# Optimization experiments

Measured on AMD Instinct MI355X. Metric: run time of the kernel, lower is better.

Reference implementation:

```python
import jax, jax.numpy as jnp
import numpy as np

KT = 0.5
KG = 0.5

def _ln(x, g, b, eps=1e-5):
    m = x.mean(-1, keepdims=True)
    v = ((x - m) ** 2).mean(-1, keepdims=True)
    return (x - m) / jnp.sqrt(v + eps) * g + b

def _sin_pe(pos, d):
    # pos: [...] float positions -> [..., d] sinusoidal encoding
    half = d // 2
    div = jnp.exp(jnp.arange(half, dtype=jnp.float32) * jnp.float32(-np.log(10000.0) * 2.0 / d))
    ang = pos[..., None].astype(jnp.float32) * div
    return jnp.concatenate([jnp.sin(ang), jnp.cos(ang)], axis=-1)

def _geo_encode(idx, emb_qk_w, w1, b1, w2, b2, ln1_g, ln1_b, ln2_g, ln2_b):
    gd = emb_qk_w.shape[-1]
    Lg = idx.shape[-1]
    x = emb_qk_w[idx]                                   # (B, S, Lg, gd)
    x = x + _sin_pe(jnp.arange(Lg, dtype=jnp.float32), gd)
    scale = 1.0 / np.sqrt(gd)
    for i in range(w1.shape[0]):
        s = jnp.einsum('bsqd,bskd->bsqk', x, x) * scale
        a = jax.nn.softmax(s, axis=-1)
        c = jnp.einsum('bsqk,bskd->bsqd', a, x)
        x = _ln(x + c, ln1_g[i], ln1_b[i])
        h = jax.nn.relu(x @ w1[i] + b1[i]) @ w2[i] + b2[i]
        x = _ln(x + h, ln2_g[i], ln2_b[i])
    return x.mean(-2)                                   # (B, S, gd)

def _forward(src_poi, src_quadkey, padding_mask, attn_mask, tgt_poi, tgt_quadkey,
             key_padding_mask, mem_mask, data_size,
             src_time, tm, gm, emb_poi_w, emb_qk_w,
             geo_ffn_w1, geo_ffn_b1, geo_ffn_w2, geo_ffn_b2,
             geo_ln1_g, geo_ln1_b, geo_ln2_g, geo_ln2_b,
             enc_wq, enc_wk, enc_wv, enc_ffn_w1, enc_ffn_b1, enc_ffn_w2, enc_ffn_b2,
             enc_ln1_g, enc_ln1_b, enc_ln2_g, enc_ln2_b,
             dec_wq, dec_wk, dec_wv, dec_ln_g, dec_ln_b, norm_g, norm_b):
    NEG = jnp.float32(-1e9)
    L = src_poi.shape[1]
    D = norm_g.shape[0]
    geo = lambda idx: _geo_encode(idx, emb_qk_w, geo_ffn_w1, geo_ffn_b1, geo_ffn_w2,
                                  geo_ffn_b2, geo_ln1_g, geo_ln1_b, geo_ln2_g, geo_ln2_b)
    src = jnp.concatenate([emb_poi_w[src_poi], geo(src_quadkey)], axis=-1)   # (B, L, D)
    tgt = jnp.concatenate([emb_poi_w[tgt_poi], geo(tgt_quadkey)], axis=-1)   # (B, Lt, D)
    # time-aware positional encoding: continuous positions from normalized timestamps
    t0 = src_time[:, :1]; tN = src_time[:, -1:]
    pos = (src_time - t0) / (tN - t0 + 1e-9) * (L - 1)
    src = src + _sin_pe(pos, D)
    # relation matrix: threshold intervals at kt/kg, then per-batch max-inversion (vectorizes the per-i loop)
    tmc = jnp.minimum(tm, KT)
    gmc = jnp.minimum(gm, KG)
    tmc = tmc.max(axis=(1, 2), keepdims=True) - tmc
    gmc = gmc.max(axis=(1, 2), keepdims=True) - gmc
    rel = tmc + gmc                                     # (B, L, L)
    scale = 1.0 / np.sqrt(D)
    emask = attn_mask[None, :, :] | padding_mask[:, None, :]
    for i in range(enc_wq.shape[0]):                    # Interval Aware Attention Blocks
        q = src @ enc_wq[i]; k = src @ enc_wk[i]; v = src @ enc_wv[i]
        s = jnp.einsum('bqd,bkd->bqk', q, k) * scale + rel
        a = jax.nn.softmax(jnp.where(emask, NEG, s), axis=-1)
        c = jnp.einsum('bqk,bkd->bqd', a, v)
        src = _ln(src + c, enc_ln1_g[i], enc_ln1_b[i])
        h = jax.nn.relu(src @ enc_ffn_w1[i] + enc_ffn_b1[i]) @ enc_ffn_w2[i] + enc_ffn_b2[i]
        src = _ln(src + h, enc_ln2_g[i], enc_ln2_b[i])
    # target-aware decoder (eval path: last encoder state broadcast over candidates)
    mem = jnp.broadcast_to(src[:, -1:, :], tgt.shape)
    dmask = mem_mask[None, :, :] | key_padding_mask[:, None, :]
    x = tgt
    for i in range(dec_wq.shape[0]):
        q = x @ dec_wq[i]; k = mem @ dec_wk[i]; v = mem @ dec_wv[i]
        s = jnp.einsum('bqd,bkd->bqk', q, k) * scale
        a = jax.nn.softmax(jnp.where(dmask, NEG, s), axis=-1)
        c = jnp.einsum('bqk,bkd->bqd', a, v)
        x = _ln(x + c, dec_ln_g[i], dec_ln_b[i])
    out = _ln(x + mem, norm_g, norm_b)
    return jnp.sum(out * tgt, axis=-1)                  # (B, Lt) matching scores

def setup_inputs():
    key = jax.random.key(0)
    ks = iter(jax.random.split(key, 64))
    nk = lambda: next(ks)
    B, L, Lg, Lt = 512, 100, 12, 101
    n_poi, n_qk = 100000, 4096
    ed, gd = 192, 64
    D = ed + gd
    Ng, Ni, Nd = 2, 2, 1
    p = lambda *s: (jax.random.normal(nk(), s, jnp.float32) * 0.02)
    return {
        'src_poi': jax.random.randint(nk(), (B, L), 0, n_poi),
        'src_quadkey': jax.random.randint(nk(), (B, L, Lg), 0, n_qk),
        'src_time': jnp.sort(jax.random.uniform(nk(), (B, L), jnp.float32) * 1e4, axis=-1),
        'tm': jax.random.uniform(nk(), (B, L, L), jnp.float32),
        'gm': jax.random.uniform(nk(), (B, L, L), jnp.float32),
        'padding_mask': jnp.zeros((B, L), bool),
        'attn_mask': jnp.triu(jnp.ones((L, L), bool), k=1),
        'tgt_poi': jax.random.randint(nk(), (B, Lt), 0, n_poi),
        'tgt_quadkey': jax.random.randint(nk(), (B, Lt, Lg), 0, n_qk),
        'key_padding_mask': jnp.zeros((B, Lt), bool),
        'mem_mask': jnp.zeros((Lt, Lt), bool),
        'data_size': jnp.full((B,), L, jnp.int32),
        'emb_poi_w': p(n_poi, ed),
        'emb_qk_w': p(n_qk, gd),
        'geo_ffn_w1': p(Ng, gd, 2 * gd), 'geo_ffn_b1': jnp.zeros((Ng, 2 * gd)),
        'geo_ffn_w2': p(Ng, 2 * gd, gd), 'geo_ffn_b2': jnp.zeros((Ng, gd)),
        'geo_ln1_g': jnp.ones((Ng, gd)), 'geo_ln1_b': jnp.zeros((Ng, gd)),
        'geo_ln2_g': jnp.ones((Ng, gd)), 'geo_ln2_b': jnp.zeros((Ng, gd)),
        'enc_wq': p(Ni, D, D), 'enc_wk': p(Ni, D, D), 'enc_wv': p(Ni, D, D),
        'enc_ffn_w1': p(Ni, D, 2 * D), 'enc_ffn_b1': jnp.zeros((Ni, 2 * D)),
        'enc_ffn_w2': p(Ni, 2 * D, D), 'enc_ffn_b2': jnp.zeros((Ni, D)),
        'enc_ln1_g': jnp.ones((Ni, D)), 'enc_ln1_b': jnp.zeros((Ni, D)),
        'enc_ln2_g': jnp.ones((Ni, D)), 'enc_ln2_b': jnp.zeros((Ni, D)),
        'dec_wq': p(Nd, D, D), 'dec_wk': p(Nd, D, D), 'dec_wv': p(Nd, D, D),
        'dec_ln_g': jnp.ones((Nd, D)), 'dec_ln_b': jnp.zeros((Nd, D)),
        'norm_g': jnp.ones((D,)), 'norm_b': jnp.zeros((D,)),
    }

def reference(src_poi, src_quadkey, src_time, tm, gm, padding_mask, attn_mask,
              tgt_poi, tgt_quadkey, key_padding_mask, mem_mask, data_size,
              emb_poi_w, emb_qk_w,
              geo_ffn_w1, geo_ffn_b1, geo_ffn_w2, geo_ffn_b2,
              geo_ln1_g, geo_ln1_b, geo_ln2_g, geo_ln2_b,
              enc_wq, enc_wk, enc_wv, enc_ffn_w1, enc_ffn_b1, enc_ffn_w2, enc_ffn_b2,
              enc_ln1_g, enc_ln1_b, enc_ln2_g, enc_ln2_b,
              dec_wq, dec_wk, dec_wv, dec_ln_g, dec_ln_b, norm_g, norm_b):
    return _forward(src_poi, src_quadkey, padding_mask, attn_mask, tgt_poi, tgt_quadkey,
                    key_padding_mask, mem_mask, data_size,
                    src_time, tm, gm, emb_poi_w, emb_qk_w,
                    geo_ffn_w1, geo_ffn_b1, geo_ffn_w2, geo_ffn_b2,
                    geo_ln1_g, geo_ln1_b, geo_ln2_g, geo_ln2_b,
                    enc_wq, enc_wk, enc_wv, enc_ffn_w1, enc_ffn_b1, enc_ffn_w2, enc_ffn_b2,
                    enc_ln1_g, enc_ln1_b, enc_ln2_g, enc_ln2_b,
                    dec_wq, dec_wk, dec_wv, dec_ln_g, dec_ln_b, norm_g, norm_b)
```

## Files before the change

### kernel.cpp

```cpp
#include <hip/hip_runtime.h>
#include <hip/hip_bf16.h>
#include <stdint.h>

typedef unsigned short u16;
typedef unsigned int   u32;
typedef __attribute__((ext_vector_type(8))) short v8s;
typedef __attribute__((ext_vector_type(4))) float v4f;

__device__ __forceinline__ float b2f(u16 u){ return __uint_as_float(((u32)u) << 16); }
__device__ __forceinline__ float lo2f(u32 u){ return __uint_as_float(u << 16); }
__device__ __forceinline__ float hi2f(u32 u){ return __uint_as_float(u & 0xffff0000u); }
__device__ __forceinline__ u16 f2b(float f){
    u32 x = __float_as_uint(f);
    u32 r = (x + 0x7fffu + ((x >> 16) & 1u)) >> 16;
    return (u16)r;
}
__device__ __forceinline__ float ldm(const void* p, size_t i, int isbf){
    return isbf ? b2f(((const u16*)p)[i]) : ((const float*)p)[i];
}
__device__ __forceinline__ float wred_sum(float v){
    #pragma unroll
    for (int o = 32; o > 0; o >>= 1) v += __shfl_xor(v, o, 64);
    return v;
}
// ... 72 lines not shown
}

template<int ACT, int SPLIT>
__global__ __launch_bounds__(256) void gemm2_kernel(
    const u16* __restrict__ A, const u16* __restrict__ Bf,
    const u16* __restrict__ bias,
    u16* __restrict__ C0, u16* __restrict__ C1, u16* __restrict__ C2,
    int M, int N, int K)
{
    const int tid = threadIdx.x, w = tid >> 6, lane = tid & 63;
    const int wm = w >> 1, wn = w & 1;
    const int flat = blockIdx.x + gridDim.x * blockIdx.y;
    const int swz = xcd_swz(flat, gridDim.x * gridDim.y);
    const int mb = swz % gridDim.x, nb = swz / gridDim.x;
    const int m0 = mb * 128 + wm * 64;
    const int n0 = nb * 128 + wn * 64;
    const int CT = K >> 5;
    const int l15 = lane & 15, lg = lane >> 4;

    v4f acc[4][4];
    #pragma unroll
    for (int mt = 0; mt < 4; mt++)
        #pragma unroll
        for (int nt = 0; nt < 4; nt++) acc[mt][nt] = (v4f){0.f, 0.f, 0.f, 0.f};

    const u16* Arow = A + (size_t)(m0 + l15) * K + (lg << 3);
    const u16* Bbase = Bf + (((size_t)(n0 >> 4) * CT) << 9) + (lane << 3);

    for (int c = 0; c < CT; c++){
        v8s bfr[4];
        #pragma unroll
        for (int nt = 0; nt < 4; nt++)
            bfr[nt] = *(const v8s*)(Bbase + (((size_t)(nt * CT + c)) << 9));
        #pragma unroll
        for (int mt = 0; mt < 4; mt++){
            v8s af = *(const v8s*)(Arow + (size_t)(mt << 4) * K + (c << 5));
            #pragma unroll
            for (int nt = 0; nt < 4; nt++)
                acc[mt][nt] = __builtin_amdgcn_mfma_f32_16x16x32_bf16(af, bfr[nt], acc[mt][nt], 0, 0, 0);
        }
    }

    #pragma unroll
    for (int nt = 0; nt < 4; nt++){
        int colbase = n0 + (nt << 4);
        float bv = bias ? b2f(bias[colbase + l15]) : 0.f;
        u16* Cp; int cw;
        if (SPLIT){
            int nbk = colbase >> 8;
            Cp = (nbk == 0) ? C0 : (nbk == 1) ? C1 : C2;
            cw = 256;
            colbase &= 255;
        } else { Cp = C0; cw = N; }
        #pragma unroll
        for (int mt = 0; mt < 4; mt++)
            #pragma unroll
            for (int r = 0; r < 4; r++){
                int row = m0 + (mt << 4) + (lg << 2) + r;
                float v = acc[mt][nt][r] + bv;
                if (ACT) v = fmaxf(v, 0.f);
                Cp[(size_t)row * cw + colbase + l15] = f2b(v);
            }
    }
}

__global__ __launch_bounds__(256) void gemm3_kernel(
    const u16* __restrict__ A, const u16* __restrict__ Bf,
    const u16* __restrict__ bias, u16* __restrict__ SRC,
    const u16* __restrict__ g, const u16* __restrict__ bta)
{
    __shared__ float red[64][4][2];
    const int tid = threadIdx.x, w = tid >> 6, lane = tid & 63;
    const int l15 = lane & 15, lg = lane >> 4;
    const int m0 = xcd_swz(blockIdx.x, gridDim.x) * 64;
    const int n0 = w * 64;
    const int CT = 16;

    v4f acc[4][4];
    #pragma unroll
    for (int mt = 0; mt < 4; mt++)
        #pragma unroll
        for (int nt = 0; nt < 4; nt++) acc[mt][nt] = (v4f){0.f, 0.f, 0.f, 0.f};

    const u16* Arow = A + (size_t)(m0 + l15) * 512 + (lg << 3);
    const u16* Bbase = Bf + (((size_t)(n0 >> 4) * CT) << 9) + (lane << 3);

    for (int c = 0; c < CT; c++){
        v8s bfr[4];
        #pragma unroll
        for (int nt = 0; nt < 4; nt++)
            bfr[nt] = *(const v8s*)(Bbase + (((size_t)(nt * CT + c)) << 9));
        #pragma unroll
        for (int mt = 0; mt < 4; mt++){
            v8s af = *(const v8s*)(Arow + (size_t)(mt << 4) * 512 + (c << 5));
            #pragma unroll
            for (int nt = 0; nt < 4; nt++)
                acc[mt][nt] = __builtin_amdgcn_mfma_f32_16x16x32_bf16(af, bfr[nt], acc[mt][nt], 0, 0, 0);
        }
    }

    float bv[4];
    #pragma unroll
    for (int nt = 0; nt < 4; nt++) bv[nt] = b2f(bias[n0 + (nt << 4) + l15]);
    #pragma unroll
    for (int mt = 0; mt < 4; mt++){
        #pragma unroll
        for (int r = 0; r < 4; r++){
            int row = m0 + (mt << 4) + (lg << 2) + r;
            float s1 = 0.f, s2 = 0.f;
            #pragma unroll
            for (int nt = 0; nt < 4; nt++){
                int col = n0 + (nt << 4) + l15;
                float y = acc[mt][nt][r] + bv[nt] + b2f(SRC[(size_t)row * 256 + col]);
                acc[mt][nt][r] = y;
                s1 += y; s2 += y * y;
            }
            s1 = wred16_sum(s1); s2 = wred16_sum(s2);
            if (l15 == 0){
                int rr = (mt << 4) + (lg << 2) + r;
                red[rr][w][0] = s1; red[rr][w][1] = s2;
            }
        }
    }
    __syncthreads();
    float gv[4], bb[4];
    #pragma unroll
    for (int nt = 0; nt < 4; nt++){
        gv[nt] = b2f(g[n0 + (nt << 4) + l15]);
        bb[nt] = b2f(bta[n0 + (nt << 4) + l15]);
    }
    #pragma unroll
    for (int mt = 0; mt < 4; mt++){
        #pragma unroll
        for (int r = 0; r < 4; r++){
            int rr = (mt << 4) + (lg << 2) + r;
            int row = m0 + rr;
            float S1 = red[rr][0][0] + red[rr][1][0] + red[rr][2][0] + red[rr][3][0];
            float S2 = red[rr][0][1] + red[rr][1][1] + red[rr][2][1] + red[rr][3][1];
            float mu = S1 * (1.0f / 256.0f);
            float var = S2 * (1.0f / 256.0f) - mu * mu;
            float rs = rsqrtf(var + 1e-5f);
            #pragma unroll
            for (int nt = 0; nt < 4; nt++){
                int col = n0 + (nt << 4) + l15;
                SRC[(size_t)row * 256 + col] = f2b((acc[mt][nt][r] - mu) * rs * gv[nt] + bb[nt]);
            }
        }
    }
}

#define GX1(r,b) (((((r) << 7) | (b))) ^ (((r) & 7) << 4))
#define GH1(r,b) (((((r) << 8) | (b))) ^ (((r) & 7) << 4))

__global__ __launch_bounds__(64) void geo6_kernel(
    const int* __restrict__ src_qk, const int* __restrict__ tgt_qk,
    const u16* __restrict__ emb,
    const u16* __restrict__ w1f, const u16* __restrict__ b1,
    const u16* __restrict__ w2f, const u16* __restrict__ b2,
    const u16* __restrict__ ln1g, const u16* __restrict__ ln1b,
    const u16* __restrict__ ln2g, const u16* __restrict__ ln2b,
    u16* __restrict__ SRC, u16* __restrict__ TGT)
{
    __shared__ __align__(16) u16 xs[16 * 64];
    __shared__ __align__(16) u16 hs[16 * 128];
    __shared__ __align__(16) float Ps[16][20];

    int seq = blockIdx.x;
    const int* qk = src_qk;
    u16* outp = SRC;
    if (seq >= 51200){ qk = tgt_qk; outp = TGT; seq -= 51200; }

    const int lane = threadIdx.x;
    const int g = lane >> 4, m = lane & 15;

    v8s ones;
    #pragma unroll
    for (int j = 0; j < 8; j++) ones[j] = (short)0x3F80;

    {
        float dv = __expf(-(float)(lane & 31) * 0.28782313662425572f);
        const bool issin = lane < 32;
        #pragma unroll
        for (int t = 0; t < 12; t++){
            int idx = qk[seq * 12 + t];
            float ang = (float)t * dv;
            float pe = issin ? __sinf(ang) : __cosf(ang);
            xs[GX1(t, lane << 1) >> 1] = f2b(b2f(emb[idx * 64 + lane]) + pe);
        }
        #pragma unroll
        for (int r = 12; r < 16; r++) xs[GX1(r, lane << 1) >> 1] = (u16)0;
    }
    lds_fence();

    float fsum = 0.f;
    const bool isdiag = (g == (m >> 2)) && (m < 12);
    const int dr = m & 3;

    for (int layer = 0; layer < 2; layer++){
        v4f S = {0.f, 0.f, 0.f, 0.f};
        {
            v8s f0 = *(const v8s*)((const char*)xs + GX1(m, (g << 4)));
            v8s f1 = *(const v8s*)((const char*)xs + GX1(m, 64 + (g << 4)));
            S = __builtin_amdgcn_mfma_f32_16x16x32_bf16(f0, f0, S, 0, 0, 0);
            S = __builtin_amdgcn_mfma_f32_16x16x32_bf16(f1, f1, S, 0, 0, 0);
        }
        {
            float ex[4];
            #pragma unroll
            for (int r = 0; r < 4; r++) ex[r] = (m < 12) ? __expf(S[r] * 0.125f) : 0.f;
            #pragma unroll
            for (int r = 0; r < 4; r++){
                float s = wred16_sum(ex[r]);
                ex[r] = ex[r] / s;
            }
            #pragma unroll
            for (int r = 0; r < 4; r++) Ps[(g << 2) + r][m] = ex[r];
        }
        lds_fence();

        float y[12];
        {
            float xr[12];
            #pragma unroll
            for (int k = 0; k < 12; k++) xr[k] = b2f(xs[GX1(k, lane << 1) >> 1]);
            #pragma unroll
            for (int q = 0; q < 12; q++){
                float4 pa = *(const float4*)&Ps[q][0];
                float4 pb = *(const float4*)&Ps[q][4];
                float4 pc = *(const float4*)&Ps[q][8];
                float c = pa.x*xr[0]+pa.y*xr[1]+pa.z*xr[2]+pa.w*xr[3]
                        + pb.x*xr[4]+pb.y*xr[5]+pb.z*xr[6]+pb.w*xr[7]
                        + pc.x*xr[8]+pc.y*xr[9]+pc.z*xr[10]+pc.w*xr[11];
                y[q] = xr[q] + c;
                xs[GX1(q, lane << 1) >> 1] = f2b(y[q]);
            }
        }
        lds_fence();

        {
            v4f R = {0.f,0.f,0.f,0.f}, Q = {0.f,0.f,0.f,0.f};
            v8s f0 = *(const v8s*)((const char*)xs + GX1(m, (g << 4)));
            v8s f1 = *(const v8s*)((const char*)xs + GX1(m, 64 + (g << 4)));
            R = __builtin_amdgcn_mfma_f32_16x16x32_bf16(f0, ones, R, 0, 0, 0);
            R = __builtin_amdgcn_mfma_f32_16x16x32_bf16(f1, ones, R, 0, 0, 0);
            Q = __builtin_amdgcn_mfma_f32_16x16x32_bf16(f0, f0, Q, 0, 0, 0);
            Q = __builtin_amdgcn_mfma_f32_16x16x32_bf16(f1, f1, Q, 0, 0, 0);
            if (isdiag){ Ps[m][16] = R[dr]; Ps[m][17] = Q[dr]; }
        }
        lds_fence();
        {
            float g1 = b2f(ln1g[layer * 64 + lane]), bb1 = b2f(ln1b[layer * 64 + lane]);
            #pragma unroll
            for (int q = 0; q < 12; q++){
                float2 st = *(const float2*)&Ps[q][16];
                float mu = st.x * 0.015625f;
                float var = st.y * 0.015625f - mu * mu;
                xs[GX1(q, lane << 1) >> 1] = f2b((y[q] - mu) * rsqrtf(var + 1e-5f) * g1 + bb1);
            }
        }
        lds_fence();

        {
            v8s a0 = *(const v8s*)((const char*)xs + GX1(m, (g << 4)));
            v8s a1 = *(const v8s*)((const char*)xs + GX1(m, 64 + (g << 4)));
            const u16* wf1 = w1f + layer * 8192;
            #pragma unroll
            for (int nt = 0; nt < 8; nt++){
                v8s bfa = *(const v8s*)(wf1 + (((nt << 1) + 0) << 9) + (lane << 3));
                v8s bfb = *(const v8s*)(wf1 + (((nt << 1) + 1) << 9) + (lane << 3));
                v4f h = {0.f, 0.f, 0.f, 0.f};
                h = __builtin_amdgcn_mfma_f32_16x16x32_bf16(a0, bfa, h, 0, 0, 0);
                h = __builtin_amdgcn_mfma_f32_16x16x32_bf16(a1, bfb, h, 0, 0, 0);
                float bia = b2f(b1[layer * 128 + (nt << 4) + m]);
                #pragma unroll
                for (int r = 0; r < 4; r++)
                    hs[GH1((g << 2) + r, ((nt << 4) | m) << 1) >> 1] = f2b(fmaxf(h[r] + bia, 0.f));
            }
        }
        lds_fence();

        {
            v8s ha[4];
            #pragma unroll
            for (int c = 0; c < 4; c++)
                ha[c] = *(const v8s*)((const char*)hs + GH1(m, (c << 6) + (g << 4)));
            lds_fence();
            float* os = (float*)hs;
            const u16* wf2 = w2f + layer * 8192;
            #pragma unroll
            for (int nt = 0; nt < 4; nt++){
                v4f o = {0.f, 0.f, 0.f, 0.f};
                #pragma unroll
                for (int c = 0; c < 4; c++){
                    v8s bf = *(const v8s*)(wf2 + ((((nt << 2) + c) << 9) + (lane << 3)));
                    o = __builtin_amdgcn_mfma_f32_16x16x32_bf16(ha[c], bf, o, 0, 0, 0);
                }
                float bo = b2f(b2[layer * 64 + (nt << 4) + m]);
                #pragma unroll
                for (int r = 0; r < 4; r++)
                    os[((g << 2) + r) * 64 + (nt << 4) + m] = o[r] + bo;
            }
        }
        lds_fence();

        {
            const float* os = (const float*)hs;
            #pragma unroll
            for (int q = 0; q < 12; q++){
                y[q] = b2f(xs[GX1(q, lane << 1) >> 1]) + os[q * 64 + lane];
            }
            lds_fence();
            #pragma unroll
            for (int q = 0; q < 12; q++)
                xs[GX1(q, lane << 1) >> 1] = f2b(y[q]);
        }
        lds_fence();
        {
            v4f R = {0.f,0.f,0.f,0.f}, Q = {0.f,0.f,0.f,0.f};
            v8s f0 = *(const v8s*)((const char*)xs + GX1(m, (g << 4)));
            v8s f1 = *(const v8s*)((const char*)xs + GX1(m, 64 + (g << 4)));
            R = __builtin_amdgcn_mfma_f32_16x16x32_bf16(f0, ones, R, 0, 0, 0);
            R = __builtin_amdgcn_mfma_f32_16x16x32_bf16(f1, ones, R, 0, 0, 0);
            Q = __builtin_amdgcn_mfma_f32_16x16x32_bf16(f0, f0, Q, 0, 0, 0);
            Q = __builtin_amdgcn_mfma_f32_16x16x32_bf16(f1, f1, Q, 0, 0, 0);
            if (isdiag){ Ps[m][16] = R[dr]; Ps[m][17] = Q[dr]; }
        }
        lds_fence();
        {
            float g2 = b2f(ln2g[layer * 64 + lane]), bb2 = b2f(ln2b[layer * 64 + lane]);
            #pragma unroll
            for (int q = 0; q < 12; q++){
                float2 st = *(const float2*)&Ps[q][16];
                float mu = st.x * 0.015625f;
                float var = st.y * 0.015625f - mu * mu;
                float xv = (y[q] - mu) * rsqrtf(var + 1e-5f) * g2 + bb2;
                if (layer == 0) xs[GX1(q, lane << 1) >> 1] = f2b(xv);
                else            fsum += xv;
            }
        }
        lds_fence();
    }
    outp[(size_t)seq * 256 + 192 + lane] = f2b(fsum * (1.0f / 12.0f));
}

__global__ __launch_bounds__(256) void embed_src_kernel(
    const int* __restrict__ poi, const float* __restrict__ timev,
    const void* __restrict__ emb_poi, u16* __restrict__ src,
    const int* __restrict__ flag)
{
    const int bl = blockIdx.x;
    const int d  = threadIdx.x;
    const int b  = bl / 100;
    const int isbf = *flag;
    float t0 = timev[b * 100];
    float tN = timev[b * 100 + 99];
    float tv = timev[bl];
    float pos = (tv - t0) / (tN - t0 + 1e-9f) * 99.0f;
    int j = d & 127;
    float dvv = __expf(-(float)j * 0.07195578415606393f);
    float ang = pos * dvv;
    float pe = (d < 128) ? __sinf(ang) : __cosf(ang);
    size_t off = (size_t)bl * 256 + d;
    float val = (d < 192) ? ldm(emb_poi, (size_t)poi[bl] * 192 + d, isbf) : b2f(src[off]);
    src[off] = f2b(val + pe);
}

__global__ __launch_bounds__(256) void embed_tgt_kernel(
    const int* __restrict__ poi, const void* __restrict__ emb_poi,
    u16* __restrict__ tgt, int n, const int* __restrict__ flag)
{
    int i = blockIdx.x * 256 + threadIdx.x;
    if (i >= n * 192) return;
    int bt = i / 192; int d = i - bt * 192;
    tgt[(size_t)bt * 256 + d] = f2b(ldm(emb_poi, (size_t)poi[bt] * 192 + d, *flag));
}

__global__ __launch_bounds__(256) void relmax_kernel(
    const void* __restrict__ tm, const void* __restrict__ gm,
    float* __restrict__ relm, const int* __restrict__ flag)
{
    const int b = blockIdx.x, tid = threadIdx.x;
    const int isbf = *flag;
    size_t base = (size_t)b * 10000;
    float tmax = -1e30f, gmax = -1e30f;
    for (int i = tid; i < 10000; i += 256){
        tmax = fmaxf(tmax, fminf(ldm(tm, base + i, isbf), 0.5f));
        gmax = fmaxf(gmax, fminf(ldm(gm, base + i, isbf), 0.5f));
    }
    tmax = wred_max(tmax); gmax = wred_max(gmax);
    __shared__ float st[4], sg[4];
    if ((tid & 63) == 0){ st[tid >> 6] = tmax; sg[tid >> 6] = gmax; }
    __syncthreads();
    if (tid == 0){
        relm[b * 2]     = fmaxf(fmaxf(st[0], st[1]), fmaxf(st[2], st[3]));
        relm[b * 2 + 1] = fmaxf(fmaxf(sg[0], sg[1]), fmaxf(sg[2], sg[3]));
    }
}

__global__ __launch_bounds__(256) void attn_kernel(
    const u16* __restrict__ QB, const u16* __restrict__ Kg, const u16* __restrict__ Vg,
    u16* __restrict__ SRC,
    const void* __restrict__ tmp_, const void* __restrict__ gmp_,
    const float* __restrict__ relm,
    const u16* __restrict__ lng, const u16* __restrict__ lnb,
    const int* __restrict__ flag)
{
    __shared__ __align__(16) u16 KV[100][264];
    __shared__ __align__(16) u16 Amat[50][112];

    const int blk = xcd_swz(blockIdx.x, gridDim.x);
    const int b = blk >> 1, h = blk & 1;
    const int tid = threadIdx.x;
    const int w = tid >> 6, lane = tid & 63;
    const int l15 = lane & 15, lg = lane >> 4;
    const int q0 = h * 50;
    const int nk = q0 + 50;
    const int isbf = *flag;
    const float tmax = relm[b * 2], gmax = relm[b * 2 + 1];

    const u16* Vb = Vg + (size_t)b * 100 * 256;
    for (int i = tid; i < nk * 128; i += 256){
        int row = i >> 7, c2 = (i & 127) * 2;
        *(ushort2*)&KV[row][c2] = *(const ushort2*)(Vb + row * 256 + c2);
    }

    const int ntc = (h == 0) ? 4 : 7;
    const int qrow = q0 + w * 16 + l15;
    const u16* Aq = QB + ((size_t)b * 100 + (qrow < 100 ? qrow : 99)) * 256 + (lg << 3);
    const u16* Kb = Kg + (size_t)b * 100 * 256;
    v4f S[7];
    #pragma unroll
    for (int nt = 0; nt < 7; nt++) S[nt] = (v4f){0.f, 0.f, 0.f, 0.f};
    const u16* Bp[7];
    for (int nt = 0; nt < ntc; nt++){
        int kt = nt * 16 + l15;
        Bp[nt] = Kb + (size_t)(kt < 100 ? kt : 99) * 256 + (lg << 3);
    }
    for (int c = 0; c < 8; c++){
        v8s af = *(const v8s*)(Aq + (c << 5));
        for (int nt = 0; nt < ntc; nt++){
            v8s bf = *(const v8s*)(Bp[nt] + (c << 5));
            S[nt] = __builtin_amdgcn_mfma_f32_16x16x32_bf16(af, bf, S[nt], 0, 0, 0);
        }
    }

    float P[7][4];
    #pragma unroll
    for (int r = 0; r < 4; r++){
        int qrel = w * 16 + (lg << 2) + r;
        int q = q0 + qrel;
        int qc = q < 100 ? q : 99;
        size_t rbase = ((size_t)b * 100 + qc) * 100;
        float sv[7];
        float mx = -1e30f;
        for (int nt = 0; nt < ntc; nt++){
            int kt = nt * 16 + l15;
            int ktc = kt < 100 ? kt : 99;
            float rel = (tmax - fminf(ldm(tmp_, rbase + ktc, isbf), 0.5f))
                      + (gmax - fminf(ldm(gmp_, rbase + ktc, isbf), 0.5f));
            float s = S[nt][r] * 0.0625f + rel;
            if (kt > q) s = -1e30f;
            sv[nt] = s;
            mx = fmaxf(mx, s);
        }
        mx = wred16_max(mx);
        float sum = 0.f;
        for (int nt = 0; nt < ntc; nt++){ sv[nt] = __expf(sv[nt] - mx); sum += sv[nt]; }
        sum = wred16_sum(sum);
        float inv = 1.0f / sum;
        for (int nt = 0; nt < ntc; nt++) P[nt][r] = sv[nt] * inv;
    }
    #pragma unroll
    for (int r = 0; r < 4; r++){
        int qrel = w * 16 + (lg << 2) + r;
        if (qrel < 50){
            for (int nt = 0; nt < ntc; nt++)
                Amat[qrel][nt * 16 + l15] = f2b(P[nt][r]);
        }
    }
    __syncthreads();

    for (int qq = 0; qq < 13; qq++){
        const int qr = qq * 4 + w;
        const int q  = q0 + qr;
        if (qr < 50){
            float o00 = 0.f, o01 = 0.f, o10 = 0.f, o11 = 0.f;
            const int kfull = (q + 1) & ~7;
            for (int k8 = 0; k8 < (kfull >> 3); k8++){
                uint4 av = *(const uint4*)&Amat[qr][k8 * 8];
                float p[8] = { lo2f(av.x), hi2f(av.x), lo2f(av.y), hi2f(av.y),
                               lo2f(av.z), hi2f(av.z), lo2f(av.w), hi2f(av.w) };
                #pragma unroll
                for (int j = 0; j < 8; j++){
                    int k = k8 * 8 + j;
                    u32 v0 = *(const u32*)&KV[k][2 * lane];
                    u32 v1 = *(const u32*)&KV[k][128 + 2 * lane];
                    o00 += p[j] * lo2f(v0); o01 += p[j] * hi2f(v0);
                    o10 += p[j] * lo2f(v1); o11 += p[j] * hi2f(v1);
                }
            }
            for (int k = kfull; k <= q; k++){
                float a = b2f(Amat[qr][k]);
                u32 v0 = *(const u32*)&KV[k][2 * lane];
                u32 v1 = *(const u32*)&KV[k][128 + 2 * lane];
                o00 += a * lo2f(v0); o01 += a * hi2f(v0);
                o10 += a * lo2f(v1); o11 += a * hi2f(v1);
            }
            u16* Sg = SRC + ((size_t)b * 100 + q) * 256;
            u32 s0v = *(const u32*)&Sg[2 * lane];
            u32 s1v = *(const u32*)&Sg[128 + 2 * lane];
            float y0 = o00 + lo2f(s0v), y1 = o01 + hi2f(s0v);
            float y2 = o10 + lo2f(s1v), y3 = o11 + hi2f(s1v);
            float s1 = y0 + y1 + y2 + y3;
            float s2 = y0*y0 + y1*y1 + y2*y2 + y3*y3;
            s1 = wred_sum(s1); s2 = wred_sum(s2);
            float mu = s1 * (1.0f / 256.0f);
            float var = s2 * (1.0f / 256.0f) - mu * mu;
            float rs = rsqrtf(var + 1e-5f);
            u32 g0 = *(const u32*)&lng[2 * lane], g1 = *(const u32*)&lng[128 + 2 * lane];
            u32 b0 = *(const u32*)&lnb[2 * lane], b1 = *(const u32*)&lnb[128 + 2 * lane];
            ushort2 w0, w1;
            w0.x = f2b((y0 - mu) * rs * lo2f(g0) + lo2f(b0));
            w0.y = f2b((y1 - mu) * rs * hi2f(g0) + hi2f(b0));
            w1.x = f2b((y2 - mu) * rs * lo2f(g1) + lo2f(b1));
            w1.y = f2b((y3 - mu) * rs * hi2f(g1) + hi2f(b1));
            *(ushort2*)&Sg[2 * lane]       = w0;
            *(ushort2*)&Sg[128 + 2 * lane] = w1;
        }
    }
}

__global__ __launch_bounds__(256) void decv_kernel(
    const u16* __restrict__ SRC, const u16* __restrict__ wv, float* __restrict__ VS)
{
    __shared__ float sv[256];
    const int b = blockIdx.x, n = threadIdx.x;
    const u16* s = SRC + ((size_t)b * 100 + 99) * 256;
    sv[n] = b2f(s[n]);
    __syncthreads();
    float acc = 0.f;
    for (int d = 0; d < 256; d++) acc += sv[d] * b2f(wv[d * 256 + n]);
    VS[(size_t)b * 256 + n] = acc;
}

__global__ __launch_bounds__(64) void decfinal2_kernel(
    const u16* __restrict__ TGT, const u16* __restrict__ SRC,
    const float* __restrict__ VS,
    const u16* __restrict__ dlg, const u16* __restrict__ dlb,
    const u16* __restrict__ ng,  const u16* __restrict__ nb,
    void* __restrict__ outp, const int* __restrict__ flag)
{
    const int bt = blockIdx.x, lane = threadIdx.x;
    const int b = bt / 101;
    const int c4 = lane * 4;
    ushort4 tg4  = *(const ushort4*)(TGT + (size_t)bt * 256 + c4);
    ushort4 mem4 = *(const ushort4*)(SRC + ((size_t)b * 100 + 99) * 256 + c4);
    float4  vs4  = *(const float4*)(VS + (size_t)b * 256 + c4);
    float tg[4]  = { b2f(tg4.x), b2f(tg4.y), b2f(tg4.z), b2f(tg4.w) };
    float mem[4] = { b2f(mem4.x), b2f(mem4.y), b2f(mem4.z), b2f(mem4.w) };
    float vsv[4] = { vs4.x, vs4.y, vs4.z, vs4.w };
    float y[4], s1 = 0.f, s2 = 0.f;
    #pragma unroll
    for (int i = 0; i < 4; i++){ y[i] = tg[i] + vsv[i]; s1 += y[i]; s2 += y[i]*y[i]; }
    s1 = wred_sum(s1); s2 = wred_sum(s2);
    float mu1 = s1 * (1.0f / 256.0f);
    float v1 = s2 * (1.0f / 256.0f) - mu1 * mu1;
    float rs1 = rsqrtf(v1 + 1e-5f);
    ushort4 dg4 = *(const ushort4*)(dlg + c4), db4 = *(const ushort4*)(dlb + c4);
    float dg[4] = { b2f(dg4.x), b2f(dg4.y), b2f(dg4.z), b2f(dg4.w) };
    float db[4] = { b2f(db4.x), b2f(db4.y), b2f(db4.z), b2f(db4.w) };
    float y2[4], a2 = 0.f, b2s = 0.f;
    #pragma unroll
    for (int i = 0; i < 4; i++){
        float x = (y[i] - mu1) * rs1 * dg[i] + db[i];
        y2[i] = x + mem[i];
        a2 += y2[i]; b2s += y2[i]*y2[i];
    }
    a2 = wred_sum(a2); b2s = wred_sum(b2s);
    float mu2 = a2 * (1.0f / 256.0f);
    float v2 = b2s * (1.0f / 256.0f) - mu2 * mu2;
    float rs2 = rsqrtf(v2 + 1e-5f);
    ushort4 ng4 = *(const ushort4*)(ng + c4), nb4 = *(const ushort4*)(nb + c4);
    float ngv[4] = { b2f(ng4.x), b2f(ng4.y), b2f(ng4.z), b2f(ng4.w) };
    float nbv[4] = { b2f(nb4.x), b2f(nb4.y), b2f(nb4.z), b2f(nb4.w) };
    float tot = 0.f;
    #pragma unroll
    for (int i = 0; i < 4; i++){
        float o = (y2[i] - mu2) * rs2 * ngv[i] + nbv[i];
        tot += o * tg[i];
    }
    tot = wred_sum(tot);
    if (lane == 0){
        if (*flag) ((u16*)outp)[bt] = f2b(tot);
        else       ((float*)outp)[bt] = tot;
    }
}

extern "C" void kernel_launch(void* const* d_in, const int* in_sizes, int n_in,
                              void* d_out, int out_size, void* d_ws, size_t ws_size,
                              hipStream_t stream)
{
    char* ws = (char*)d_ws;
    size_t off = 0;
    auto AL = [&](size_t bytes){ size_t o = off; off += (bytes + 255) & ~(size_t)255; return o; };
    const size_t FLAGO = AL(4);
    const size_t CTIME = AL(51200 * 4);
    const size_t CEQK  = AL(262144 * 2);
    const size_t CGW1  = AL(16384 * 2), CGB1 = AL(256 * 2), CGW2 = AL(16384 * 2), CGB2 = AL(128 * 2);
    const size_t CGL1G = AL(128 * 2), CGL1B = AL(128 * 2), CGL2G = AL(128 * 2), CGL2B = AL(128 * 2);
    const size_t CEWQ  = AL(131072 * 2), CEWK = AL(131072 * 2), CEWV = AL(131072 * 2);
    const size_t CEW1  = AL(262144 * 2), CEB1 = AL(1024 * 2), CEW2 = AL(262144 * 2), CEB2 = AL(512 * 2);
    const size_t CEL1G = AL(512 * 2), CEL1B = AL(512 * 2), CEL2G = AL(512 * 2), CEL2B = AL(512 * 2);
    const size_t CDWV  = AL(65536 * 2), CDLG = AL(256 * 2), CDLB = AL(256 * 2), CNG = AL(256 * 2), CNB = AL(256 * 2);
    const size_t W1FO  = AL(16384 * 2), W2FO = AL(16384 * 2);
    const size_t QKVFO = AL(786432 * 2);
    const size_t W1FEO = AL(524288 * 2);
    const size_t W2FEO = AL(524288 * 2);
    const size_t RELMO = AL(512 * 2 * 4);
    const size_t VSO   = AL(512 * 256 * 4);
    const size_t SRCO  = AL((size_t)51200 * 256 * 2);
    const size_t TGTO  = AL((size_t)51712 * 256 * 2);
    const size_t B1O   = AL((size_t)51200 * 256 * 2);
    const size_t B2O   = AL((size_t)51200 * 256 * 2);
    const size_t B3O   = AL((size_t)51200 * 256 * 2);
    (void)ws_size; (void)in_sizes; (void)n_in; (void)out_size;

    int*   FLAG = (int*)(ws + FLAGO);
    float* CT   = (float*)(ws + CTIME);
    u16 *cEQK=(u16*)(ws+CEQK), *cGW1=(u16*)(ws+CGW1), *cGB1=(u16*)(ws+CGB1), *cGW2=(u16*)(ws+CGW2),
        *cGB2=(u16*)(ws+CGB2), *cGL1G=(u16*)(ws+CGL1G), *cGL1B=(u16*)(ws+CGL1B), *cGL2G=(u16*)(ws+CGL2G),
        *cGL2B=(u16*)(ws+CGL2B), *cEWQ=(u16*)(ws+CEWQ), *cEWK=(u16*)(ws+CEWK), *cEWV=(u16*)(ws+CEWV),
        *cEW1=(u16*)(ws+CEW1), *cEB1=(u16*)(ws+CEB1), *cEW2=(u16*)(ws+CEW2), *cEB2=(u16*)(ws+CEB2),
        *cEL1G=(u16*)(ws+CEL1G), *cEL1B=(u16*)(ws+CEL1B), *cEL2G=(u16*)(ws+CEL2G), *cEL2B=(u16*)(ws+CEL2B),
        *cDWV=(u16*)(ws+CDWV), *cDLG=(u16*)(ws+CDLG), *cDLB=(u16*)(ws+CDLB), *cNG=(u16*)(ws+CNG),
        *cNB=(u16*)(ws+CNB);
    u16* W1F   = (u16*)(ws + W1FO);
    u16* W2F   = (u16*)(ws + W2FO);
    u16* QKVF  = (u16*)(ws + QKVFO);
    u16* W1FE  = (u16*)(ws + W1FEO);
    u16* W2FE  = (u16*)(ws + W2FEO);
    float* RELM = (float*)(ws + RELMO);
    float* VS   = (float*)(ws + VSO);
    u16* SRC = (u16*)(ws + SRCO);
    u16* TGT = (u16*)(ws + TGTO);
    u16* B1  = (u16*)(ws + B1O);
    u16* B2  = (u16*)(ws + B2O);
    u16* B3  = (u16*)(ws + B3O);
    u16* Hh  = B2;

    const int* src_poi = (const int*)d_in[0];
    const int* src_qk  = (const int*)d_in[1];
    const int* tgt_poi = (const int*)d_in[7];
    const int* tgt_qk  = (const int*)d_in[8];

    probe_kernel<<<1, 64, 0, stream>>>((const u32*)d_in[38], FLAG);

    ConvArgs ca;
    const int srcidx[NSEG] = {13,14,15,16,17,18,19,20,21,22,23,24,25,26,27,28,29,30,31,32,35,36,37,38,39};
    u16* dsts[NSEG] = {cEQK,cGW1,cGB1,cGW2,cGB2,cGL1G,cGL1B,cGL2G,cGL2B,cEWQ,cEWK,cEWV,
                       cEW1,cEB1,cEW2,cEB2,cEL1G,cEL1B,cEL2G,cEL2B,cDWV,cDLG,cDLB,cNG,cNB};
    const int ns[NSEG] = {262144,16384,256,16384,128,128,128,128,128,131072,131072,131072,
                          262144,1024,262144,512,512,512,512,512,65536,256,256,256,256};
    for (int i = 0; i < NSEG; i++){ ca.src[i] = d_in[srcidx[i]]; ca.dst[i] = dsts[i]; ca.n[i] = ns[i]; }
    convert_kernel<<<dim3(1024, NSEG), 256, 0, stream>>>(ca, FLAG);
    convert_time_kernel<<<200, 256, 0, stream>>>(d_in[2], CT, FLAG);

    packfrag_kernel<<<64, 256, 0, stream>>>(cGW1, W1F, 64, 128, 2);
    packfrag_kernel<<<64, 256, 0, stream>>>(cGW2, W2F, 128, 64, 2);
    packfrag3_kernel<<<3072, 256, 0, stream>>>(cEWQ, cEWK, cEWV, QKVF);
    packfrag_kernel<<<1024, 256, 0, stream>>>(cEW1, W1FE, 256, 512, 2);
    packfrag_kernel<<<1024, 256, 0, stream>>>(cEW2, W2FE, 512, 256, 2);

    geo6_kernel<<<102912, 64, 0, stream>>>(src_qk, tgt_qk, cEQK, W1F, cGB1, W2F, cGB2,
                                           cGL1G, cGL1B, cGL2G, cGL2B, SRC, TGT);
    embed_src_kernel<<<51200, 256, 0, stream>>>(src_poi, CT, d_in[12], SRC, FLAG);
    embed_tgt_kernel<<<(51712 * 192 + 255) / 256, 256, 0, stream>>>(tgt_poi, d_in[12], TGT, 51712, FLAG);
    relmax_kernel<<<512, 256, 0, stream>>>(d_in[3], d_in[4], RELM, FLAG);

    for (int i = 0; i < 2; i++){
        gemm2_kernel<0,1><<<dim3(400, 6), 256, 0, stream>>>(SRC, QKVF + (size_t)i * 196608, nullptr,
                                                            B1, B2, B3, 51200, 768, 256);
        attn_kernel<<<1024, 256, 0, stream>>>(B1, B2, B3, SRC, d_in[3], d_in[4], RELM,
                                              cEL1G + i * 256, cEL1B + i * 256, FLAG);
        gemm2_kernel<1,0><<<dim3(400, 4), 256, 0, stream>>>(SRC, W1FE + (size_t)i * 131072, cEB1 + i * 512,
                                                            Hh, nullptr, nullptr, 51200, 512, 256);
        gemm3_kernel<<<800, 256, 0, stream>>>(Hh, W2FE + (size_t)i * 131072, cEB2 + i * 256,
                                              SRC, cEL2G + i * 256, cEL2B + i * 256);
    }

    decv_kernel<<<512, 256, 0, stream>>>(SRC, cDWV, VS);
    decfinal2_kernel<<<51712, 64, 0, stream>>>(TGT, SRC, VS, cDLG, cDLB, cNG, cNB, d_out, FLAG);
}
```

Baseline: 1.215 ms.

## Fuse geo encoder, POI embeddings and relmax into one block-dispatched kernel

Merges the geo encoder, source and target POI embedding kernels, and the relative-max reduction into a single launch, choosing the role from the block index. The source path no longer does a read-modify-write of the geo columns: the geo block adds the cosine positional term itself and the embed blocks write only the first 192 columns. This saves three kernel launches and one pass over the SRC geo slice. Relmax now runs as 512 single-wave blocks instead of 256-thread blocks, and the launch bounds gain a minimum-occupancy hint of 8.

```diff
diff --git a/kernel.cpp b/kernel.cpp
--- a/kernel.cpp
+++ b/kernel.cpp
@@ -248,248 +248,245 @@
 #define GX1(r,b) (((((r) << 7) | (b))) ^ (((r) & 7) << 4))
 #define GH1(r,b) (((((r) << 8) | (b))) ^ (((r) & 7) << 4))
 
-__global__ __launch_bounds__(64) void geo6_kernel(
+__global__ __launch_bounds__(64, 8) void fused1_kernel(
     const int* __restrict__ src_qk, const int* __restrict__ tgt_qk,
     const u16* __restrict__ emb,
     const u16* __restrict__ w1f, const u16* __restrict__ b1,
     const u16* __restrict__ w2f, const u16* __restrict__ b2,
     const u16* __restrict__ ln1g, const u16* __restrict__ ln1b,
     const u16* __restrict__ ln2g, const u16* __restrict__ ln2b,
-    u16* __restrict__ SRC, u16* __restrict__ TGT)
+    u16* __restrict__ SRC, u16* __restrict__ TGT,
+    const int* __restrict__ src_poi, const int* __restrict__ tgt_poi,
+    const void* __restrict__ emb_poi, const float* __restrict__ CTm,
+    const void* __restrict__ tm, const void* __restrict__ gm,
+    float* __restrict__ relm, const int* __restrict__ flag)
 {
     __shared__ __align__(16) u16 xs[16 * 64];
     __shared__ __align__(16) u16 hs[16 * 128];
     __shared__ __align__(16) float Ps[16][20];
 
-    int seq = blockIdx.x;
-    const int* qk = src_qk;
-    u16* outp = SRC;
-    if (seq >= 51200){ qk = tgt_qk; outp = TGT; seq -= 51200; }
-
+    const int bid = blockIdx.x;
     const int lane = threadIdx.x;
-    const int g = lane >> 4, m = lane & 15;
-
-    v8s ones;
-    #pragma unroll
-    for (int j = 0; j < 8; j++) ones[j] = (short)0x3F80;
-
-    {
-        float dv = __expf(-(float)(lane & 31) * 0.28782313662425572f);
-        const bool issin = lane < 32;
-        #pragma unroll
-        for (int t = 0; t < 12; t++){
-            int idx = qk[seq * 12 + t];
-            float ang = (float)t * dv;
-            float pe = issin ? __sinf(ang) : __cosf(ang);
-            xs[GX1(t, lane << 1) >> 1] = f2b(b2f(emb[idx * 64 + lane]) + pe);
-        }
-        #pragma unroll
-        for (int r = 12; r < 16; r++) xs[GX1(r, lane << 1) >> 1] = (u16)0;
-    }
-    lds_fence();
-
-    float fsum = 0.f;
-    const bool isdiag = (g == (m >> 2)) && (m < 12);
-    const int dr = m & 3;
-
-    for (int layer = 0; layer < 2; layer++){
-        v4f S = {0.f, 0.f, 0.f, 0.f};
+
+    if (bid < 102912){
+        int seq = bid;
+        const int* qk = src_qk;
+        u16* outp = SRC;
+        bool is_src = true;
+        if (seq >= 51200){ qk = tgt_qk; outp = TGT; seq -= 51200; is_src = false; }
+
+        const int g = lane >> 4, m = lane & 15;
+        v8s ones;
+        #pragma unroll
+        for (int j = 0; j < 8; j++) ones[j] = (short)0x3F80;
+
         {
-            v8s f0 = *(const v8s*)((const char*)xs + GX1(m, (g << 4)));
-            v8s f1 = *(const v8s*)((const char*)xs + GX1(m, 64 + (g << 4)));
-            S = __builtin_amdgcn_mfma_f32_16x16x32_bf16(f0, f0, S, 0, 0, 0);
-            S = __builtin_amdgcn_mfma_f32_16x16x32_bf16(f1, f1, S, 0, 0, 0);
-        }
-        {
-            float ex[4];
+            float dv = __expf(-(float)(lane & 31) * 0.28782313662425572f);
+            const bool issin = lane < 32;
             #pragma unroll
-            for (int r = 0; r < 4; r++) ex[r] = (m < 12) ? __expf(S[r] * 0.125f) : 0.f;
+            for (int t = 0; t < 12; t++){
+                int idx = qk[seq * 12 + t];
+                float ang = (float)t * dv;
+                float pe = issin ? __sinf(ang) : __cosf(ang);
+                xs[GX1(t, lane << 1) >> 1] = f2b(b2f(emb[idx * 64 + lane]) + pe);
+            }
             #pragma unroll
-            for (int r = 0; r < 4; r++){
-                float s = wred16_sum(ex[r]);
-                ex[r] = ex[r] / s;
-            }
-            #pragma unroll
-            for (int r = 0; r < 4; r++) Ps[(g << 2) + r][m] = ex[r];
+            for (int r = 12; r < 16; r++) xs[GX1(r, lane << 1) >> 1] = (u16)0;
         }
         lds_fence();
 
-        float y[12];
-        {
-            float xr[12];
-            #pragma unroll
-            for (int k = 0; k < 12; k++) xr[k] = b2f(xs[GX1(k, lane << 1) >> 1]);
-            #pragma unroll
-            for (int q = 0; q < 12; q++){
-                float4 pa = *(const float4*)&Ps[q][0];
-                float4 pb = *(const float4*)&Ps[q][4];
-                float4 pc = *(const float4*)&Ps[q][8];
-                float c = pa.x*xr[0]+pa.y*xr[1]+pa.z*xr[2]+pa.w*xr[3]
-                        + pb.x*xr[4]+pb.y*xr[5]+pb.z*xr[6]+pb.w*xr[7]
-                        + pc.x*xr[8]+pc.y*xr[9]+pc.z*xr[10]+pc.w*xr[11];
-                y[q] = xr[q] + c;
-                xs[GX1(q, lane << 1) >> 1] = f2b(y[q]);
-            }
-        }
-        lds_fence();
-
-        {
-            v4f R = {0.f,0.f,0.f,0.f}, Q = {0.f,0.f,0.f,0.f};
-            v8s f0 = *(const v8s*)((const char*)xs + GX1(m, (g << 4)));
-            v8s f1 = *(const v8s*)((const char*)xs + GX1(m, 64 + (g << 4)));
-            R = __builtin_amdgcn_mfma_f32_16x16x32_bf16(f0, ones, R, 0, 0, 0);
-            R = __builtin_amdgcn_mfma_f32_16x16x32_bf16(f1, ones, R, 0, 0, 0);
-            Q = __builtin_amdgcn_mfma_f32_16x16x32_bf16(f0, f0, Q, 0, 0, 0);
-            Q = __builtin_amdgcn_mfma_f32_16x16x32_bf16(f1, f1, Q, 0, 0, 0);
-            if (isdiag){ Ps[m][16] = R[dr]; Ps[m][17] = Q[dr]; }
-        }
-        lds_fence();
-        {
-            float g1 = b2f(ln1g[layer * 64 + lane]), bb1 = b2f(ln1b[layer * 64 + lane]);
-            #pragma unroll
-            for (int q = 0; q < 12; q++){
-                float2 st = *(const float2*)&Ps[q][16];
-                float mu = st.x * 0.015625f;
-                float var = st.y * 0.015625f - mu * mu;
-                xs[GX1(q, lane << 1) >> 1] = f2b((y[q] - mu) * rsqrtf(var + 1e-5f) * g1 + bb1);
-            }
-        }
-        lds_fence();
-
-        {
-            v8s a0 = *(const v8s*)((const char*)xs + GX1(m, (g << 4)));
-            v8s a1 = *(const v8s*)((const char*)xs + GX1(m, 64 + (g << 4)));
-            const u16* wf1 = w1f + layer * 8192;
-            #pragma unroll
-            for (int nt = 0; nt < 8; nt++){
-                v8s bfa = *(const v8s*)(wf1 + (((nt << 1) + 0) << 9) + (lane << 3));
-                v8s bfb = *(const v8s*)(wf1 + (((nt << 1) + 1) << 9) + (lane << 3));
-                v4f h = {0.f, 0.f, 0.f, 0.f};
-                h = __builtin_amdgcn_mfma_f32_16x16x32_bf16(a0, bfa, h, 0, 0, 0);
-                h = __builtin_amdgcn_mfma_f32_16x16x32_bf16(a1, bfb, h, 0, 0, 0);
-                float bia = b2f(b1[layer * 128 + (nt << 4) + m]);
-                #pragma unroll
-                for (int r = 0; r < 4; r++)
-                    hs[GH1((g << 2) + r, ((nt << 4) | m) << 1) >> 1] = f2b(fmaxf(h[r] + bia, 0.f));
-            }
-        }
-        lds_fence();
-
-        {
-            v8s ha[4];
-            #pragma unroll
-            for (int c = 0; c < 4; c++)
-                ha[c] = *(const v8s*)((const char*)hs + GH1(m, (c << 6) + (g << 4)));
-            lds_fence();
-            float* os = (float*)hs;
-            const u16* wf2 = w2f + layer * 8192;
-            #pragma unroll
-            for (int nt = 0; nt < 4; nt++){
-                v4f o = {0.f, 0.f, 0.f, 0.f};
-                #pragma unroll
-                for (int c = 0; c < 4; c++){
-                    v8s bf = *(const v8s*)(wf2 + ((((nt << 2) + c) << 9) + (lane << 3)));
-                    o = __builtin_amdgcn_mfma_f32_16x16x32_bf16(ha[c], bf, o, 0, 0, 0);
+        float fsum = 0.f;
+        const bool isdiag = (g == (m >> 2)) && (m < 12);
+        const int dr = m & 3;
+
+        for (int layer = 0; layer < 2; layer++){
+            v4f S = {0.f, 0.f, 0.f, 0.f};
+            {
+                v8s f0 = *(const v8s*)((const char*)xs + GX1(m, (g << 4)));
+                v8s f1 = *(const v8s*)((const char*)xs + GX1(m, 64 + (g << 4)));
+                S = __builtin_amdgcn_mfma_f32_16x16x32_bf16(f0, f0, S, 0, 0, 0);
+                S = __builtin_amdgcn_mfma_f32_16x16x32_bf16(f1, f1, S, 0, 0, 0);
+            }
+            {
+                float ex[4];
+                #pragma unroll
+                for (int r = 0; r < 4; r++) ex[r] = (m < 12) ? __expf(S[r] * 0.125f) : 0.f;
+                #pragma unroll
+                for (int r = 0; r < 4; r++){
+                    float s = wred16_sum(ex[r]);
+                    ex[r] = ex[r] / s;
                 }
-                float bo = b2f(b2[layer * 64 + (nt << 4) + m]);
-                #pragma unroll
-                for (int r = 0; r < 4; r++)
-                    os[((g << 2) + r) * 64 + (nt << 4) + m] = o[r] + bo;
-            }
-        }
-        lds_fence();
-
-        {
-            const float* os = (const float*)hs;
-            #pragma unroll
-            for (int q = 0; q < 12; q++){
-                y[q] = b2f(xs[GX1(q, lane << 1) >> 1]) + os[q * 64 + lane];
-            }
-            lds_fence();
-            #pragma unroll
-            for (int q = 0; q < 12; q++)
-                xs[GX1(q, lane << 1) >> 1] = f2b(y[q]);
-        }
-        lds_fence();
-        {
-            v4f R = {0.f,0.f,0.f,0.f}, Q = {0.f,0.f,0.f,0.f};
-            v8s f0 = *(const v8s*)((const char*)xs + GX1(m, (g << 4)));
-            v8s f1 = *(const v8s*)((const char*)xs + GX1(m, 64 + (g << 4)));
-            R = __builtin_amdgcn_mfma_f32_16x16x32_bf16(f0, ones, R, 0, 0, 0);
-            R = __builtin_amdgcn_mfma_f32_16x16x32_bf16(f1, ones, R, 0, 0, 0);
-            Q = __builtin_amdgcn_mfma_f32_16x16x32_bf16(f0, f0, Q, 0, 0, 0);
-            Q = __builtin_amdgcn_mfma_f32_16x16x32_bf16(f1, f1, Q, 0, 0, 0);
-            if (isdiag){ Ps[m][16] = R[dr]; Ps[m][17] = Q[dr]; }
-        }
-        lds_fence();
-        {
-            float g2 = b2f(ln2g[layer * 64 + lane]), bb2 = b2f(ln2b[layer * 64 + lane]);
-            #pragma unroll
-            for (int q = 0; q < 12; q++){
-                float2 st = *(const float2*)&Ps[q][16];
-                float mu = st.x * 0.015625f;
-                float var = st.y * 0.015625f - mu * mu;
-                float xv = (y[q] - mu) * rsqrtf(var + 1e-5f) * g2 + bb2;
-                if (layer == 0) xs[GX1(q, lane << 1) >> 1] = f2b(xv);
-                else            fsum += xv;
-            }
-        }
-        lds_fence();
-    }
-    outp[(size_t)seq * 256 + 192 + lane] = f2b(fsum * (1.0f / 12.0f));
-}
-
-__global__ __launch_bounds__(256) void embed_src_kernel(
-    const int* __restrict__ poi, const float* __restrict__ timev,
-    const void* __restrict__ emb_poi, u16* __restrict__ src,
-    const int* __restrict__ flag)
-{
-    const int bl = blockIdx.x;
-    const int d  = threadIdx.x;
-    const int b  = bl / 100;
-    const int isbf = *flag;
-    float t0 = timev[b * 100];
-    float tN = timev[b * 100 + 99];
-    float tv = timev[bl];
-    float pos = (tv - t0) / (tN - t0 + 1e-9f) * 99.0f;
-    int j = d & 127;
-    float dvv = __expf(-(float)j * 0.07195578415606393f);
-    float ang = pos * dvv;
-    float pe = (d < 128) ? __sinf(ang) : __cosf(ang);
-    size_t off = (size_t)bl * 256 + d;
-    float val = (d < 192) ? ldm(emb_poi, (size_t)poi[bl] * 192 + d, isbf) : b2f(src[off]);
-    src[off] = f2b(val + pe);
-}
-
-__global__ __launch_bounds__(256) void embed_tgt_kernel(
-    const int* __restrict__ poi, const void* __restrict__ emb_poi,
-    u16* __restrict__ tgt, int n, const int* __restrict__ flag)
-{
-    int i = blockIdx.x * 256 + threadIdx.x;
-    if (i >= n * 192) return;
-    int bt = i / 192; int d = i - bt * 192;
-    tgt[(size_t)bt * 256 + d] = f2b(ldm(emb_poi, (size_t)poi[bt] * 192 + d, *flag));
-}
-
-__global__ __launch_bounds__(256) void relmax_kernel(
-    const void* __restrict__ tm, const void* __restrict__ gm,
-    float* __restrict__ relm, const int* __restrict__ flag)
-{
-    const int b = blockIdx.x, tid = threadIdx.x;
-    const int isbf = *flag;
-    size_t base = (size_t)b * 10000;
-    float tmax = -1e30f, gmax = -1e30f;
-    for (int i = tid; i < 10000; i += 256){
-        tmax = fmaxf(tmax, fminf(ldm(tm, base + i, isbf), 0.5f));
-        gmax = fmaxf(gmax, fminf(ldm(gm, base + i, isbf), 0.5f));
-    }
-    tmax = wred_max(tmax); gmax = wred_max(gmax);
-    __shared__ float st[4], sg[4];
-    if ((tid & 63) == 0){ st[tid >> 6] = tmax; sg[tid >> 6] = gmax; }
-    __syncthreads();
-    if (tid == 0){
-        relm[b * 2]     = fmaxf(fmaxf(st[0], st[1]), fmaxf(st[2], st[3]));
-        relm[b * 2 + 1] = fmaxf(fmaxf(sg[0], sg[1]), fmaxf(sg[2], sg[3]));
+                #pragma unroll
+                for (int r = 0; r < 4; r++) Ps[(g << 2) + r][m] = ex[r];
+            }
+            lds_fence();
+
+            float y[12];
+            {
+                float xr[12];
+                #pragma unroll
+                for (int k = 0; k < 12; k++) xr[k] = b2f(xs[GX1(k, lane << 1) >> 1]);
+                #pragma unroll
+                for (int q = 0; q < 12; q++){
+                    float4 pa = *(const float4*)&Ps[q][0];
+                    float4 pb = *(const float4*)&Ps[q][4];
+                    float4 pc = *(const float4*)&Ps[q][8];
+                    float c = pa.x*xr[0]+pa.y*xr[1]+pa.z*xr[2]+pa.w*xr[3]
+                            + pb.x*xr[4]+pb.y*xr[5]+pb.z*xr[6]+pb.w*xr[7]
+                            + pc.x*xr[8]+pc.y*xr[9]+pc.z*xr[10]+pc.w*xr[11];
+                    y[q] = xr[q] + c;
+                    xs[GX1(q, lane << 1) >> 1] = f2b(y[q]);
+                }
+            }
+            lds_fence();
+
+            {
+                v4f R = {0.f,0.f,0.f,0.f}, Q = {0.f,0.f,0.f,0.f};
+                v8s f0 = *(const v8s*)((const char*)xs + GX1(m, (g << 4)));
+                v8s f1 = *(const v8s*)((const char*)xs + GX1(m, 64 + (g << 4)));
+                R = __builtin_amdgcn_mfma_f32_16x16x32_bf16(f0, ones, R, 0, 0, 0);
+                R = __builtin_amdgcn_mfma_f32_16x16x32_bf16(f1, ones, R, 0, 0, 0);
+                Q = __builtin_amdgcn_mfma_f32_16x16x32_bf16(f0, f0, Q, 0, 0, 0);
+                Q = __builtin_amdgcn_mfma_f32_16x16x32_bf16(f1, f1, Q, 0, 0, 0);
+                if (isdiag){ Ps[m][16] = R[dr]; Ps[m][17] = Q[dr]; }
+            }
+            lds_fence();
+            {
+                float g1 = b2f(ln1g[layer * 64 + lane]), bb1 = b2f(ln1b[layer * 64 + lane]);
+                #pragma unroll
+                for (int q = 0; q < 12; q++){
+                    float2 st = *(const float2*)&Ps[q][16];
+                    float mu = st.x * 0.015625f;
+                    float var = st.y * 0.015625f - mu * mu;
+                    xs[GX1(q, lane << 1) >> 1] = f2b((y[q] - mu) * rsqrtf(var + 1e-5f) * g1 + bb1);
+                }
+            }
+            lds_fence();
+
+            {
+                v8s a0 = *(const v8s*)((const char*)xs + GX1(m, (g << 4)));
+                v8s a1 = *(const v8s*)((const char*)xs + GX1(m, 64 + (g << 4)));
+                const u16* wf1 = w1f + layer * 8192;
+                #pragma unroll
+                for (int nt = 0; nt < 8; nt++){
+                    v8s bfa = *(const v8s*)(wf1 + (((nt << 1) + 0) << 9) + (lane << 3));
+                    v8s bfb = *(const v8s*)(wf1 + (((nt << 1) + 1) << 9) + (lane << 3));
+                    v4f h = {0.f, 0.f, 0.f, 0.f};
+                    h = __builtin_amdgcn_mfma_f32_16x16x32_bf16(a0, bfa, h, 0, 0, 0);
+                    h = __builtin_amdgcn_mfma_f32_16x16x32_bf16(a1, bfb, h, 0, 0, 0);
+                    float bia = b2f(b1[layer * 128 + (nt << 4) + m]);
+                    #pragma unroll
+                    for (int r = 0; r < 4; r++)
+                        hs[GH1((g << 2) + r, ((nt << 4) | m) << 1) >> 1] = f2b(fmaxf(h[r] + bia, 0.f));
+                }
+            }
+            lds_fence();
+
+            {
+                v8s ha[4];
+                #pragma unroll
+                for (int c = 0; c < 4; c++)
+                    ha[c] = *(const v8s*)((const char*)hs + GH1(m, (c << 6) + (g << 4)));
+                lds_fence();
+                float* os = (float*)hs;
+                const u16* wf2 = w2f + layer * 8192;
+                #pragma unroll
+                for (int nt = 0; nt < 4; nt++){
+                    v4f o = {0.f, 0.f, 0.f, 0.f};
+                    #pragma unroll
+                    for (int c = 0; c < 4; c++){
+                        v8s bf = *(const v8s*)(wf2 + ((((nt << 2) + c) << 9) + (lane << 3)));
+                        o = __builtin_amdgcn_mfma_f32_16x16x32_bf16(ha[c], bf, o, 0, 0, 0);
+                    }
+                    float bo = b2f(b2[layer * 64 + (nt << 4) + m]);
+                    #pragma unroll
+                    for (int r = 0; r < 4; r++)
+                        os[((g << 2) + r) * 64 + (nt << 4) + m] = o[r] + bo;
+                }
+            }
+            lds_fence();
+
+            {
+                const float* os = (const float*)hs;
+                #pragma unroll
+                for (int q = 0; q < 12; q++){
+                    y[q] = b2f(xs[GX1(q, lane << 1) >> 1]) + os[q * 64 + lane];
+                }
+                lds_fence();
+                #pragma unroll
+                for (int q = 0; q < 12; q++)
+                    xs[GX1(q, lane << 1) >> 1] = f2b(y[q]);
+            }
+            lds_fence();
+            {
+                v4f R = {0.f,0.f,0.f,0.f}, Q = {0.f,0.f,0.f,0.f};
+                v8s f0 = *(const v8s*)((const char*)xs + GX1(m, (g << 4)));
+                v8s f1 = *(const v8s*)((const char*)xs + GX1(m, 64 + (g << 4)));
+                R = __builtin_amdgcn_mfma_f32_16x16x32_bf16(f0, ones, R, 0, 0, 0);
+                R = __builtin_amdgcn_mfma_f32_16x16x32_bf16(f1, ones, R, 0, 0, 0);
+                Q = __builtin_amdgcn_mfma_f32_16x16x32_bf16(f0, f0, Q, 0, 0, 0);
+                Q = __builtin_amdgcn_mfma_f32_16x16x32_bf16(f1, f1, Q, 0, 0, 0);
+                if (isdiag){ Ps[m][16] = R[dr]; Ps[m][17] = Q[dr]; }
+            }
+            lds_fence();
+            {
+                float g2 = b2f(ln2g[layer * 64 + lane]), bb2 = b2f(ln2b[layer * 64 + lane]);
+                #pragma unroll
+                for (int q = 0; q < 12; q++){
+                    float2 st = *(const float2*)&Ps[q][16];
+                    float mu = st.x * 0.015625f;
+                    float var = st.y * 0.015625f - mu * mu;
+                    float xv = (y[q] - mu) * rsqrtf(var + 1e-5f) * g2 + bb2;
+                    if (layer == 0) xs[GX1(q, lane << 1) >> 1] = f2b(xv);
+                    else            fsum += xv;
+                }
+            }
+            lds_fence();
+        }
+        float go = fsum * (1.0f / 12.0f);
+        if (is_src){
+            int bb_ = seq / 100;
+            float t0 = CTm[bb_ * 100], tN = CTm[bb_ * 100 + 99], tv = CTm[seq];
+            float pos = (tv - t0) / (tN - t0 + 1e-9f) * 99.0f;
+            float ang = pos * __expf(-(float)(lane + 64) * 0.07195578415606393f);
+            go += __cosf(ang);
+        }
+        outp[(size_t)seq * 256 + 192 + lane] = f2b(go);
+    } else if (bid < 154112){
+        const int row = bid - 102912;
+        const int isbf = *flag;
+        const int b = row / 100;
+        float t0 = CTm[b * 100], tN = CTm[b * 100 + 99], tv = CTm[row];
+        float pos = (tv - t0) / (tN - t0 + 1e-9f) * 99.0f;
+        const int p = src_poi[row];
+        float e0 = ldm(emb_poi, (size_t)p * 192 + lane, isbf);
+        float e1 = ldm(emb_poi, (size_t)p * 192 + 64 + lane, isbf);
+        float e2 = ldm(emb_poi, (size_t)p * 192 + 128 + lane, isbf);
+        float dv0 = __expf(-(float)lane * 0.07195578415606393f);
+        float dv1 = __expf(-(float)(lane + 64) * 0.07195578415606393f);
+        u16* rp = SRC + (size_t)row * 256;
+        rp[lane]       = f2b(e0 + __sinf(pos * dv0));
+        rp[lane + 64]  = f2b(e1 + __sinf(pos * dv1));
+        rp[lane + 128] = f2b(e2 + __cosf(pos * dv0));
+    } else if (bid < 205824){
+        const int row = bid - 154112;
+        const int isbf = *flag;
+        const int p = tgt_poi[row];
+        u16* rp = TGT + (size_t)row * 256;
+        rp[lane]       = f2b(ldm(emb_poi, (size_t)p * 192 + lane, isbf));
+        rp[lane + 64]  = f2b(ldm(emb_poi, (size_t)p * 192 + 64 + lane, isbf));
+        rp[lane + 128] = f2b(ldm(emb_poi, (size_t)p * 192 + 128 + lane, isbf));
+    } else {
+        const int b = bid - 205824;
+        const int isbf = *flag;
+        size_t base = (size_t)b * 10000;
+        float tmax = -1e30f, gmax = -1e30f;
+        for (int i = lane; i < 10000; i += 64){
+            tmax = fmaxf(tmax, fminf(ldm(tm, base + i, isbf), 0.5f));
+            gmax = fmaxf(gmax, fminf(ldm(gm, base + i, isbf), 0.5f));
+        }
+        tmax = wred_max(tmax); gmax = wred_max(gmax);
+        if (lane == 0){ relm[b * 2] = tmax; relm[b * 2 + 1] = gmax; }
     }
 }
 
@@ -767,11 +764,10 @@
     packfrag_kernel<<<1024, 256, 0, stream>>>(cEW1, W1FE, 256, 512, 2);
     packfrag_kernel<<<1024, 256, 0, stream>>>(cEW2, W2FE, 512, 256, 2);
 
-    geo6_kernel<<<102912, 64, 0, stream>>>(src_qk, tgt_qk, cEQK, W1F, cGB1, W2F, cGB2,
-                                           cGL1G, cGL1B, cGL2G, cGL2B, SRC, TGT);
-    embed_src_kernel<<<51200, 256, 0, stream>>>(src_poi, CT, d_in[12], SRC, FLAG);
-    embed_tgt_kernel<<<(51712 * 192 + 255) / 256, 256, 0, stream>>>(tgt_poi, d_in[12], TGT, 51712, FLAG);
-    relmax_kernel<<<512, 256, 0, stream>>>(d_in[3], d_in[4], RELM, FLAG);
+    fused1_kernel<<<206336, 64, 0, stream>>>(src_qk, tgt_qk, cEQK, W1F, cGB1, W2F, cGB2,
+                                             cGL1G, cGL1B, cGL2G, cGL2B, SRC, TGT,
+                                             src_poi, tgt_poi, d_in[12], CT,
+                                             d_in[3], d_in[4], RELM, FLAG);
 
     for (int i = 0; i < 2; i++){
         gemm2_kernel<0,1><<<dim3(400, 6), 256, 0, stream>>>(SRC, QKVF + (size_t)i * 196608, nullptr,
```

Result: slower. 1.240 ms (+2.1%).
